# Kernel tuning notes

Measured on AMD Instinct MI355X. Metric: run time of the kernel, lower is better.

Reference implementation:

```python
import jax, jax.numpy as jnp
import numpy as np

B, L, G, N, K, E = 64, 512, 128, 32, 8, 65536
NTOK, D_TOK, H_DIR, NTL_INP, NHID, NREL = 10000, 64, 64, 32, 16, 16


def _bn(x, gamma, beta, eps=1e-5):
    # training-mode BatchNorm1d over axis 0; x: (n, C)
    mu = x.mean(0)
    var = x.var(0)
    return gamma * (x - mu) / jnp.sqrt(var + eps) + beta


def _lstm(x, w_ih, w_hh, b_ih, b_hh):
    # x: (B, T, D); torch gate order i, f, g, o
    nb = x.shape[0]
    H = w_hh.shape[1]
    def step(carry, xt):
        h, c = carry
        g = xt @ w_ih.T + b_ih + h @ w_hh.T + b_hh
        i, f, gg, o = jnp.split(g, 4, axis=-1)
        c = jax.nn.sigmoid(f) * c + jax.nn.sigmoid(i) * jnp.tanh(gg)
        h = jax.nn.sigmoid(o) * jnp.tanh(c)
        return (h, c), h
    init = (jnp.zeros((nb, H), x.dtype), jnp.zeros((nb, H), x.dtype))
    _, hs = jax.lax.scan(step, init, jnp.swapaxes(x, 0, 1))
    return jnp.swapaxes(hs, 0, 1)


def setup_inputs() -> dict:
    key = jax.random.key(0)
    ks = jax.random.split(key, 24)
    inp = {}
    inp['seq'] = jax.random.randint(ks[0], (B, L), 0, NTOK)
    inp['pos2grp'] = jax.random.randint(ks[1], (B, L), 0, G)
    inp['idx'] = jax.random.randint(ks[2], (B, N, K), 0, L)
    inp['u'] = jax.random.randint(ks[3], (E,), 0, B * N)
    inp['v'] = jax.random.randint(ks[4], (E,), 0, B * N)
    # parameters
    s = 1.0 / np.sqrt(H_DIR)
    inp['tok_emb'] = jax.random.normal(ks[5], (NTOK, D_TOK), jnp.float32)
    for tag, k0 in (('f', 6), ('b', 10)):
        inp[f'w_ih_{tag}'] = s * jax.random.normal(ks[k0], (4 * H_DIR, D_TOK), jnp.float32)
        inp[f'w_hh_{tag}'] = s * jax.random.normal(ks[k0 + 1], (4 * H_DIR, H_DIR), jnp.float32)
        inp[f'b_ih_{tag}'] = s * jax.random.normal(ks[k0 + 2], (4 * H_DIR,), jnp.float32)
        inp[f'b_hh_{tag}'] = s * jax.random.normal(ks[k0 + 3], (4 * H_DIR,), jnp.float32)
    inp['w_src'] = (1.0 / np.sqrt(2 * H_DIR)) * jax.random.normal(ks[14], (NTL_INP, 2 * H_DIR), jnp.float32)
    inp['b_src'] = jnp.zeros((NTL_INP,), jnp.float32)
    inp['w_dst'] = (1.0 / np.sqrt(2 * H_DIR)) * jax.random.normal(ks[15], (NTL_INP, 2 * H_DIR), jnp.float32)
    inp['b_dst'] = jnp.zeros((NTL_INP,), jnp.float32)
    inp['g_src'] = jnp.ones((NTL_INP,), jnp.float32)
    inp['be_src'] = jnp.zeros((NTL_INP,), jnp.float32)
    inp['g_dst'] = jnp.ones((NTL_INP,), jnp.float32)
    inp['be_dst'] = jnp.zeros((NTL_INP,), jnp.float32)
    inp['ntl_w'] = 0.001 * jax.random.normal(ks[16], (NREL, NHID, NTL_INP, NTL_INP), jnp.float32)
    inp['ntl_v'] = 0.001 * jax.random.normal(ks[17], (NREL, NHID, 2 * NTL_INP), jnp.float32)
    inp['ntl_b'] = jnp.zeros((NREL, NHID, 1), jnp.float32)
    inp['ntl_u'] = 0.001 * jax.random.normal(ks[18], (NREL, 1, NHID), jnp.float32)
    inp['ntl_g'] = jnp.ones((NREL * NHID,), jnp.float32)
    inp['ntl_be'] = jnp.zeros((NREL * NHID,), jnp.float32)
    return inp


def reference(seq, pos2grp, idx, u, v, tok_emb,
              w_ih_f, w_hh_f, b_ih_f, b_hh_f,
              w_ih_b, w_hh_b, b_ih_b, b_hh_b,
              w_src, b_src, w_dst, b_dst,
              g_src, be_src, g_dst, be_dst,
              ntl_w, ntl_v, ntl_b, ntl_u, ntl_g, ntl_be):
    # token embed + scatter-sum tokens -> groups
    x_tok = tok_emb[seq]                                   # (B, L, D)
    gid = (pos2grp + jnp.arange(B)[:, None] * G).reshape(-1)
    x_grp = jax.ops.segment_sum(x_tok.reshape(B * L, -1), gid,
                                num_segments=B * G).reshape(B, G, -1)
    # bidirectional LSTM over groups
    hf = _lstm(x_grp, w_ih_f, w_hh_f, b_ih_f, b_hh_f)
    hb = jnp.flip(_lstm(jnp.flip(x_grp, 1), w_ih_b, w_hh_b, b_ih_b, b_hh_b), 1)
    h_grp = jnp.concatenate([hf, hb], -1)                  # (B, G, 2H)
    # hierarchical gather + sum: node <- sum over K token positions' groups
    b_idx = jnp.arange(B)[:, None, None]
    g_idx = pos2grp[b_idx, idx]                            # (B, N, K)
    h = h_grp[b_idx, g_idx].sum(2).reshape(B * N, -1)      # (B*N, 2H)
    # edge endpoint projections + batchnorm
    hs = _bn(h[u] @ w_src.T + b_src, g_src, be_src)        # (E, ninp)
    ht = _bn(h[v] @ w_dst.T + b_dst, g_dst, be_dst)
    # Neural Tensor Layer
    linear = jnp.einsum('rhd,nd->rhn', ntl_v, jnp.concatenate([hs, ht], 1))
    bil = jnp.stack([
        jnp.einsum('nhj,nj->hn', jnp.einsum('ni,hij->nhj', hs, ntl_w[r]), ht)
        for r in range(NREL)], 0)                          # (R, H, E)
    z = bil + linear + ntl_b
    mu = z.mean(-1, keepdims=True)
    var = z.var(-1, keepdims=True)
    zn = ntl_g.reshape(NREL, NHID, 1) * (z - mu) / jnp.sqrt(var + 1e-5) \
         + ntl_be.reshape(NREL, NHID, 1)
    t = jnp.tanh(zn)
    logit = jnp.einsum('rh,rhn->nr', ntl_u[:, 0, :], t)    # (E, R)
    return logit
```

## Files before the change

### kernel.cpp

```cpp
#include <hip/hip_runtime.h>
#include <hip/hip_bf16.h>
#include <cstdint>

constexpr int B_   = 64;
constexpr int L_   = 512;
constexpr int G_   = 128;
constexpr int E_   = 65536;
constexpr int RH   = 256;
constexpr int M_   = 2048;
constexpr int JA   = 33;
constexpr int COLS = RH * JA;
constexpr int STRD = 36;
constexpr int K_   = 8;

#define DEV static __device__ __forceinline__

DEV float sigm(float x) { return 1.f / (1.f + __expf(-x)); }
DEV float tanh_fast(float x) {
    x = fminf(15.f, fmaxf(-15.f, x));
    float e = __expf(2.f * x);
    return (e - 1.f) / (e + 1.f);
}
DEV int rfl(int x) { return __builtin_amdgcn_readfirstlane(x); }

__global__ __launch_bounds__(256) void k_eh(const int* __restrict__ seq,
                                            const int* __restrict__ p2g,
                                            const float* __restrict__ emb,
                                            const int* __restrict__ u,
                                            const int* __restrict__ v,
                                            float* __restrict__ xg,
                                            int* __restrict__ cu, int* __restrict__ cv) {
    int blk = blockIdx.x;
    int t   = threadIdx.x;
    if (blk >= 64) {
        int n = (blk - 64) * 256 + t;
        atomicAdd(&cu[u[n]], 1);
        atomicAdd(&cv[v[n]], 1);
        return;
    }
    __shared__ float xgl[G_ * 64];
    for (int i = t; i < G_ * 64; i += 256) xgl[i] = 0.f;
    __syncthreads();
    int b = blk;
    int d = t & 63, part = t >> 6;
#pragma unroll 8
    for (int l = part; l < L_; l += 4) {
        int s = seq[b * L_ + l];
        int g = p2g[b * L_ + l];
        atomicAdd(&xgl[g * 64 + d], emb[s * 64 + d]);
    }
    __syncthreads();
    for (int i = t; i < G_ * 64; i += 256) xg[(size_t)b * G_ * 64 + i] = xgl[i];
}

__global__ __launch_bounds__(256) void k_pre(const float* __restrict__ xg,
                                             const float* __restrict__ wihf,
                                             const float* __restrict__ bihf,
                                             const float* __restrict__ bhhf,
                                             const float* __restrict__ wihb,
                                             const float* __restrict__ bihb,
                                             const float* __restrict__ bhhb,
                                             float* __restrict__ pre,
                                             const int* __restrict__ cu,
                                             int* __restrict__ ustart,
                                             int* __restrict__ ucursor) {
    int blk = blockIdx.x;
    int t   = threadIdx.x;
    if (blk == 512) {
        __shared__ int ps[256];
        int base = t * 8, run = 0;
        int c[8], loc[8];
#pragma unroll
        for (int i = 0; i < 8; i++) c[i] = cu[base + i];
#pragma unroll
        for (int i = 0; i < 8; i++) { loc[i] = run; run += c[i]; }
        ps[t] = run;
        __syncthreads();
        for (int off = 1; off < 256; off <<= 1) {
            int a = (t >= off) ? ps[t - off] : 0;
            __syncthreads();
            ps[t] += a;
            __syncthreads();
        }
        int ex = ps[t] - run;
#pragma unroll
        for (int i = 0; i < 8; i++) { ustart[base + i] = ex + loc[i]; ucursor[base + i] = ex + loc[i]; }
        if (t == 255) ustart[2048] = E_;
        return;
    }
    int dir = blk >> 8;
    const float* wih = dir ? wihb : wihf;
    float bias = dir ? (bihb[t] + bhhb[t]) : (bihf[t] + bhhf[t]);
    int r0 = (blk & 255) * 32;

    float4 wv[16];
#pragma unroll
    for (int c = 0; c < 16; c++) wv[c] = ((const float4*)(wih + t * 64))[c];

#pragma unroll 2
    for (int ml = 0; ml < 32; ml++) {
        const float* xr = xg + (size_t)(r0 + ml) * 64;
        float acc = bias;
#pragma unroll
        for (int c = 0; c < 16; c++) {
            float x0 = xr[4 * c], x1 = xr[4 * c + 1], x2 = xr[4 * c + 2], x3 = xr[4 * c + 3];
            acc += x0 * wv[c].x + x1 * wv[c].y + x2 * wv[c].z + x3 * wv[c].w;
        }
        pre[((size_t)dir * 8192 + r0 + ml) * 256 + t] = acc;
    }
}

__global__ __launch_bounds__(256, 1) void k_lstm(const float* __restrict__ pre,
                                                 const float* __restrict__ whh_f,
                                                 const float* __restrict__ whh_b,
                                                 float* __restrict__ hgrp,
                                                 const int* __restrict__ u,
                                                 const int* __restrict__ v,
                                                 int* __restrict__ ucursor,
                                                 int2* __restrict__ eonv) {
    int blk = blockIdx.x;
    int t   = threadIdx.x;
    if (blk >= 128) {
        int n = (blk - 128) * 256 + t;
        int pos = atomicAdd(&ucursor[u[n]], 1);
        eonv[pos] = make_int2(n, v[n]);
        return;
    }
    __shared__ __align__(16) float plds[64][256];
    __shared__ __align__(16) float hl[2][64];
    __shared__ float gl[256];
    int dir = blk >> 6;
    int b   = blk & 63;
    const float* whh = dir ? whh_b : whh_f;
    const float* src = pre + ((size_t)dir * 8192 + (size_t)b * G_) * 256;

    float4 wv[16];
#pragma unroll
    for (int c = 0; c < 16; c++) wv[c] = ((const float4*)(whh + t * 64))[c];

    {
        int base = dir ? 64 : 0;
        const float4* s4 = (const float4*)(src + (size_t)base * 256);
        float4* d4 = (float4*)&plds[0][0];
#pragma unroll
        for (int i = 0; i < 16; i++) d4[i * 256 + t] = s4[i * 256 + t];
    }
    if (t < 64) hl[0][t] = 0.f;
    float creg = 0.f;
    __syncthreads();
    int q = t >> 6;

    for (int half = 0; half < 2; half++) {
        if (half == 1) {
            int base = dir ? 0 : 64;
            const float4* s4 = (const float4*)(src + (size_t)base * 256);
            float4* d4 = (float4*)&plds[0][0];
#pragma unroll
            for (int i = 0; i < 16; i++) d4[i * 256 + t] = s4[i * 256 + t];
            __syncthreads();
        }
        for (int kk = 0; kk < 64; kk++) {
            int k = half * 64 + kk;
            int s = dir ? (G_ - 1 - k) : k;
            float p = plds[s & 63][t];
            const float4* hp = (const float4*)hl[k & 1];
            float a0 = p, a1 = 0.f, a2 = 0.f, a3 = 0.f;
#pragma unroll
            for (int c = 0; c < 16; c += 4) {
                float4 h0 = hp[c], h1 = hp[c + 1], h2 = hp[c + 2], h3 = hp[c + 3];
                a0 += h0.x * wv[c].x     + h0.y * wv[c].y     + h0.z * wv[c].z     + h0.w * wv[c].w;
                a1 += h1.x * wv[c + 1].x + h1.y * wv[c + 1].y + h1.z * wv[c + 1].z + h1.w * wv[c + 1].w;
                a2 += h2.x * wv[c + 2].x + h2.y * wv[c + 2].y + h2.z * wv[c + 2].z + h2.w * wv[c + 2].w;
                a3 += h3.x * wv[c + 3].x + h3.y * wv[c + 3].y + h3.z * wv[c + 3].z + h3.w * wv[c + 3].w;
            }
            float g = (a0 + a1) + (a2 + a3);
            gl[t] = (q == 2) ? tanh_fast(g) : sigm(g);
            __syncthreads();
            if (t < 64) {
                float ai = gl[t], af = gl[64 + t], ag = gl[128 + t], ao = gl[192 + t];
                float c2 = af * creg + ai * ag;
                float hh = ao * tanh_fast(c2);
                creg = c2;
                hl[(k + 1) & 1][t] = hh;
                hgrp[((size_t)(b * G_ + s)) * 128 + dir * 64 + t] = hh;
            }
            __syncthreads();
        }
    }
}

__global__ __launch_bounds__(128) void k_gather(const int* __restrict__ idx,
                                                const int* __restrict__ p2g,
                                                const float* __restrict__ hgrp,
                                                float* __restrict__ hnode) {
    int m = blockIdx.x;
    int d = threadIdx.x;
    int b = m >> 5;
    float acc = 0.f;
#pragma unroll
    for (int k = 0; k < K_; k++) {
        int l = idx[m * K_ + k];
        int g = p2g[b * L_ + l];
        acc += hgrp[((size_t)b * G_ + g) * 128 + d];
    }
    hnode[(size_t)m * 128 + d] = acc;
}

__global__ __launch_bounds__(256) void k_proj(const float* __restrict__ hnode,
                                              const float* __restrict__ wsrc,
                                              const float* __restrict__ bsrc,
                                              const float* __restrict__ wdst,
                                              const float* __restrict__ bdst,
                                              float* __restrict__ Ps, float* __restrict__ Pd) {
    int m0 = blockIdx.x * 8;
    int t  = threadIdx.x;
    int ml = t >> 5, o = t & 31;
    float4 sw[32], dw[32];
#pragma unroll
    for (int c = 0; c < 32; c++) {
        sw[c] = ((const float4*)(wsrc + (size_t)o * 128))[c];
        dw[c] = ((const float4*)(wdst + (size_t)o * 128))[c];
    }
    const float* hr = hnode + (size_t)(m0 + ml) * 128;
    float accS = bsrc[o], accD = bdst[o];
#pragma unroll
    for (int c = 0; c < 32; c++) {
        float x0 = hr[4 * c], x1 = hr[4 * c + 1], x2 = hr[4 * c + 2], x3 = hr[4 * c + 3];
        accS += x0 * sw[c].x + x1 * sw[c].y + x2 * sw[c].z + x3 * sw[c].w;
        accD += x0 * dw[c].x + x1 * dw[c].y + x2 * dw[c].z + x3 * dw[c].w;
    }
    Ps[(size_t)(m0 + ml) * 32 + o] = accS;
    Pd[(size_t)(m0 + ml) * 32 + o] = accD;
}

__global__ __launch_bounds__(256) void k_bnstat(const float* __restrict__ Ps,
                                                 const float* __restrict__ Pd,
                                                 const int* __restrict__ cu,
                                                 const int* __restrict__ cv,
                                                 float* __restrict__ bn_raw) {
    int side = blockIdx.x & 1, sl = blockIdx.x >> 1;
    const float* P  = side ? Pd : Ps;
    const int*   cn = side ? cv : cu;
    int t = threadIdx.x;
    int mp = t >> 5, o = t & 31;
    float s1 = 0.f, s2 = 0.f;
#pragma unroll
    for (int i = 0; i < 8; i++) {
        int m = sl * 64 + i * 8 + mp;
        float c = (float)cn[m];
        float x = P[(size_t)m * 32 + o];
        s1 += c * x;
        s2 += c * x * x;
    }
    __shared__ float r1[256], r2[256];
    r1[t] = s1; r2[t] = s2;
    __syncthreads();
    for (int off = 128; off >= 32; off >>= 1) {
        if (t < off) { r1[t] += r1[t + off]; r2[t] += r2[t + off]; }
        __syncthreads();
    }
    if (t < 32) {
        atomicAdd(&bn_raw[side * 64 + t], r1[t]);
        atomicAdd(&bn_raw[side * 64 + 32 + t], r2[t]);
    }
}

__global__ __launch_bounds__(256) void k_prep(const float* __restrict__ Ps,
                                              const float* __restrict__ Pd,
                                              const float* __restrict__ bn_raw,
                                              const float* __restrict__ gs,
                                              const float* __restrict__ bes,
                                              const float* __restrict__ gd,
                                              const float* __restrict__ bed,
                                              const float* __restrict__ ntlw,
                                              const float* __restrict__ ntlv,
                                              const float* __restrict__ ntlb,
                                              float* __restrict__ hsaug,
                                              float* __restrict__ htaug,
                                              float* __restrict__ waug) {
    int blk = blockIdx.x;
    int t   = threadIdx.x;
    constexpr float invE = 1.f / (float)E_;
    if (blk < 576) {
        int gid = blk * 256 + t;
        int m = gid / (2 * STRD), s2 = gid % (2 * STRD);
        if (s2 < STRD) {
            int i = s2;
            float val = 0.f;
            if (i < 32) {
                float mu  = bn_raw[i] * invE;
                float isd = rsqrtf(bn_raw[32 + i] * invE - mu * mu + 1e-5f);
                val = gs[i] * (Ps[(size_t)m * 32 + i] - mu) * isd + bes[i];
            } else if (i == 32) val = 1.f;
            hsaug[(size_t)m * STRD + i] = val;
        } else {
            int j = s2 - STRD;
            float val = 0.f;
            if (j < 32) {
                float mu  = bn_raw[64 + j] * invE;
                float isd = rsqrtf(bn_raw[96 + j] * invE - mu * mu + 1e-5f);
                val = gd[j] * (Pd[(size_t)m * 32 + j] - mu) * isd + bed[j];
            } else if (j == 32) val = 1.f;
            htaug[(size_t)m * STRD + j] = val;
        }
        return;
    }
    int gid = (blk - 576) * 256 + t;
    int i   = gid / COLS;
    int rem = gid - i * COLS;
    int rh  = rem / JA;
    int j   = rem - rh * JA;
    float val;
    if (i < 32) val = (j < 32) ? ntlw[((size_t)rh * 32 + i) * 32 + j] : ntlv[rh * 64 + i];
    else        val = (j < 32) ? ntlv[rh * 64 + 32 + j] : ntlb[rh];
    waug[(size_t)i * COLS + j * 256 + rh] = val;
}

__global__ __launch_bounds__(256) void k_agemm(const float* __restrict__ hsaug,
                                               const float* __restrict__ waug,
                                               __hip_bfloat16* __restrict__ A) {
    int mt = blockIdx.x;
    int j  = blockIdx.y;
    int t  = threadIdx.x;
    float w[JA];
#pragma unroll
    for (int i = 0; i < JA; i++) w[i] = waug[(size_t)i * COLS + j * 256 + t];

#pragma unroll 2
    for (int ml = 0; ml < 32; ml++) {
        const float* hr = hsaug + (size_t)(mt * 32 + ml) * STRD;
        float a0 = 0.f, a1 = 0.f;
#pragma unroll
        for (int i = 0; i < 32; i += 2) {
            a0 += hr[i] * w[i];
            a1 += hr[i + 1] * w[i + 1];
        }
        float acc = a0 + a1 + hr[32] * w[32];
        A[(size_t)(mt * 32 + ml) * COLS + j * 256 + t] = __float2bfloat16(acc);
    }
}

DEV void load_ht(float* d, const float* __restrict__ htaug, int vv) {
    const float* hp = htaug + (size_t)vv * STRD;
#pragma unroll
    for (int j = 0; j < JA; j++) d[j] = hp[j];
}
DEV void edge_compute(const float* av, const float* ht, int n, int t,
                      __hip_bfloat16* __restrict__ z, float& s1, float& s2) {
    float a0 = 0.f, a1 = 0.f;
#pragma unroll
    for (int j = 0; j < 32; j += 2) {
        a0 += av[j] * ht[j];
        a1 += av[j + 1] * ht[j + 1];
    }
    float acc = a0 + a1 + av[32] * ht[32];
    z[(size_t)n * 256 + t] = __float2bfloat16(acc);
    s1 += acc; s2 += acc * acc;
}

__global__ __launch_bounds__(256) void k_z(const __hip_bfloat16* __restrict__ A,
                                           const float* __restrict__ htaug,
                                           const int* __restrict__ ustart,
                                           const int2* __restrict__ eonv,
                                           __hip_bfloat16* __restrict__ z,
                                           float* __restrict__ zsum,
                                           float* __restrict__ zsq) {
    int t = threadIdx.x;
    float s1 = 0.f, s2 = 0.f;
    for (int ui = 0; ui < 4; ui++) {
        int uu = blockIdx.x * 4 + ui;
        float av[JA];
#pragma unroll
        for (int j = 0; j < JA; j++)
            av[j] = __bfloat162float(A[(size_t)uu * COLS + j * 256 + t]);
        int e0 = ustart[uu], e1 = ustart[uu + 1];
        if (e0 >= e1) continue;
        int e = e0;
        int2 q0 = eonv[e];
        int n0 = rfl(q0.x), v0 = rfl(q0.y);
        float ht0[JA]; load_ht(ht0, htaug, v0);
        int n1 = 0, v1 = 0; float ht1[JA];
        while (true) {
            if (e + 1 < e1) {
                int2 q = eonv[e + 1];
                n1 = rfl(q.x); v1 = rfl(q.y);
                load_ht(ht1, htaug, v1);
            }
            edge_compute(av, ht0, n0, t, z, s1, s2);
            if (++e >= e1) break;
            if (e + 1 < e1) {
                int2 q = eonv[e + 1];
                n0 = rfl(q.x); v0 = rfl(q.y);
                load_ht(ht0, htaug, v0);
            }
            edge_compute(av, ht1, n1, t, z, s1, s2);
            if (++e >= e1) break;
        }
    }
    atomicAdd(&zsum[t], s1);
    atomicAdd(&zsq[t], s2);
}

__global__ __launch_bounds__(256) void k_logit(const __hip_bfloat16* __restrict__ z,
                                               const float* __restrict__ zsum,
                                               const float* __restrict__ zsq,
                                               const float* __restrict__ ntlu,
                                               const float* __restrict__ ntlg,
                                               const float* __restrict__ ntlbe,
                                               float* __restrict__ out) {
    int t  = threadIdx.x;
    int n0 = blockIdx.x * 16;
    float mu  = zsum[t] / (float)E_;
    float var = zsq[t] / (float)E_ - mu * mu;
    float isd = rsqrtf(var + 1e-5f);
    float g   = ntlg[t],  be  = ntlbe[t];
    float uw  = ntlu[t];
    float zv[16];
#pragma unroll
    for (int nl = 0; nl < 16; nl++)
        zv[nl] = __bfloat162float(z[(size_t)(n0 + nl) * 256 + t]);
#pragma unroll 1
    for (int nl = 0; nl < 16; nl++) {
        float zn  = g * (zv[nl] - mu) * isd + be;
        float val = uw * tanh_fast(zn);
        val += __shfl_xor(val, 1);
        val += __shfl_xor(val, 2);
        val += __shfl_xor(val, 4);
        val += __shfl_xor(val, 8);
        if ((t & 15) == 0) out[(size_t)(n0 + nl) * 16 + (t >> 4)] = val;
    }
}

extern "C" void kernel_launch(void* const* d_in, const int* in_sizes, int n_in,
                              void* d_out, int out_size, void* d_ws, size_t ws_size,
                              hipStream_t stream) {
    const int*   seq   = (const int*)d_in[0];
    const int*   p2g   = (const int*)d_in[1];
    const int*   idx   = (const int*)d_in[2];
    const int*   u     = (const int*)d_in[3];
    const int*   v     = (const int*)d_in[4];
    const float* emb   = (const float*)d_in[5];
    const float* wihf  = (const float*)d_in[6];
    const float* whhf  = (const float*)d_in[7];
    const float* bihf  = (const float*)d_in[8];
    const float* bhhf  = (const float*)d_in[9];
    const float* wihb  = (const float*)d_in[10];
    const float* whhb  = (const float*)d_in[11];
    const float* bihb  = (const float*)d_in[12];
    const float* bhhb  = (const float*)d_in[13];
    const float* wsrc  = (const float*)d_in[14];
    const float* bsrc  = (const float*)d_in[15];
    const float* wdst  = (const float*)d_in[16];
    const float* bdst  = (const float*)d_in[17];
    const float* gs    = (const float*)d_in[18];
    const float* bes   = (const float*)d_in[19];
    const float* gd    = (const float*)d_in[20];
    const float* bed   = (const float*)d_in[21];
    const float* ntlw  = (const float*)d_in[22];
    const float* ntlv  = (const float*)d_in[23];
    const float* ntlb  = (const float*)d_in[24];
    const float* ntlu  = (const float*)d_in[25];
    const float* ntlg  = (const float*)d_in[26];
    const float* ntlbe = (const float*)d_in[27];
    float* out = (float*)d_out;

    char* ws = (char*)d_ws;
    size_t off = 0;
    auto take = [&](size_t bytes) -> char* {
        char* p = ws + off;
        off = (off + bytes + 255) & ~(size_t)255;
        return p;
    };
    int*   cnt_u  = (int*)  take(2048 * 4);
    int*   cnt_v  = (int*)  take(2048 * 4);
    float* zsum   = (float*)take(256 * 4);
    float* zsq    = (float*)take(256 * 4);
    float* bn_raw = (float*)take(128 * 4);
    size_t zero_bytes = off;
    float* x_grp   = (float*)take((size_t)B_ * G_ * 64 * 4);
    int*   ucursor = (int*)  take(2048 * 4);
    int*   ustart  = (int*)  take(2049 * 4);
    int2*  eonv    = (int2*) take((size_t)E_ * 8);
    float* pre     = (float*)take((size_t)2 * 8192 * 256 * 4);
    float* hgrp    = (float*)take((size_t)B_ * G_ * 128 * 4);
    float* hnode   = (float*)take((size_t)M_ * 128 * 4);
    float* Psrc    = (float*)take((size_t)M_ * 32 * 4);
    float* Pdst    = (float*)take((size_t)M_ * 32 * 4);
    float* hsaug   = (float*)take((size_t)M_ * STRD * 4);
    float* htaug   = (float*)take((size_t)M_ * STRD * 4);
    float* waug    = (float*)take((size_t)JA * COLS * 4);
    __hip_bfloat16* Abuf = (__hip_bfloat16*)take((size_t)M_ * COLS * 2);
    __hip_bfloat16* zbuf = (__hip_bfloat16*)take((size_t)E_ * 256 * 2);
    (void)ws_size; (void)in_sizes; (void)n_in; (void)out_size;

    hipMemsetAsync(d_ws, 0, zero_bytes, stream);

    k_eh<<<320, 256, 0, stream>>>(seq, p2g, emb, u, v, x_grp, cnt_u, cnt_v);
    k_pre<<<513, 256, 0, stream>>>(x_grp, wihf, bihf, bhhf, wihb, bihb, bhhb, pre,
                                   cnt_u, ustart, ucursor);
    k_lstm<<<384, 256, 0, stream>>>(pre, whhf, whhb, hgrp, u, v, ucursor, eonv);
    k_gather<<<M_, 128, 0, stream>>>(idx, p2g, hgrp, hnode);
    k_proj<<<M_ / 8, 256, 0, stream>>>(hnode, wsrc, bsrc, wdst, bdst, Psrc, Pdst);
    k_bnstat<<<64, 256, 0, stream>>>(Psrc, Pdst, cnt_u, cnt_v, bn_raw);
    k_prep<<<576 + 1089, 256, 0, stream>>>(Psrc, Pdst, bn_raw, gs, bes, gd, bed,
                                           ntlw, ntlv, ntlb, hsaug, htaug, waug);
    k_agemm<<<dim3(64, JA), 256, 0, stream>>>(hsaug, waug, Abuf);
    k_z<<<M_ / 4, 256, 0, stream>>>(Abuf, htaug, ustart, eonv, zbuf, zsum, zsq);
    k_logit<<<E_ / 16, 256, 0, stream>>>(zbuf, zsum, zsq, ntlu, ntlg, ntlbe, out);
}
```

Measured before the change: 428.9 us.

## Redo LSTM recurrence with lane broadcasts, fuse gather/proj/bnstat, widen k_z grid

The LSTM step now keeps h in registers and broadcasts it with readlane instead of going through LDS. Each wave redundantly computes the cell update, which removes the second barrier per step, and the h history is buffered in LDS then written out per half. The gather, projection and BN-statistics kernels are merged into one kernel that keeps the node rows in shared memory, removing the hnode round trip and two launches. k_z now launches one block per source node instead of four, giving more parallelism at the cost of more blocks and more per-block atomics.

```diff
diff --git a/kernel.cpp b/kernel.cpp
--- a/kernel.cpp
+++ b/kernel.cpp
@@ -11,7 +11,6 @@
 constexpr int JA   = 33;
 constexpr int COLS = RH * JA;
 constexpr int STRD = 36;
-constexpr int K_   = 8;
 
 #define DEV static __device__ __forceinline__
 
@@ -22,6 +21,9 @@
     return (e - 1.f) / (e + 1.f);
 }
 DEV int rfl(int x) { return __builtin_amdgcn_readfirstlane(x); }
+DEV float rdlane(float x, int lane) {
+    return __int_as_float(__builtin_amdgcn_readlane(__float_as_int(x), lane));
+}
 
 __global__ __launch_bounds__(256) void k_eh(const int* __restrict__ seq,
                                             const int* __restrict__ p2g,
@@ -127,141 +129,135 @@
         return;
     }
     __shared__ __align__(16) float plds[64][256];
-    __shared__ __align__(16) float hl[2][64];
-    __shared__ float gl[256];
+    __shared__ __align__(16) float hist[64][64];
+    __shared__ float gl[2][256];
     int dir = blk >> 6;
     int b   = blk & 63;
     const float* whh = dir ? whh_b : whh_f;
     const float* src = pre + ((size_t)dir * 8192 + (size_t)b * G_) * 256;
+    int e = t & 63;
+    int q = t >> 6;
 
     float4 wv[16];
 #pragma unroll
-    for (int c = 0; c < 16; c++) wv[c] = ((const float4*)(whh + t * 64))[c];
-
-    {
-        int base = dir ? 64 : 0;
-        const float4* s4 = (const float4*)(src + (size_t)base * 256);
-        float4* d4 = (float4*)&plds[0][0];
-#pragma unroll
-        for (int i = 0; i < 16; i++) d4[i * 256 + t] = s4[i * 256 + t];
-    }
-    if (t < 64) hl[0][t] = 0.f;
-    float creg = 0.f;
-    __syncthreads();
-    int q = t >> 6;
+    for (int c = 0; c < 16; c++) wv[c] = ((const float4*)(whh + (size_t)t * 64))[c];
+
+    float h = 0.f, creg = 0.f;
 
     for (int half = 0; half < 2; half++) {
-        if (half == 1) {
-            int base = dir ? 0 : 64;
+        {
+            int base = (dir ^ half) ? 64 : 0;
             const float4* s4 = (const float4*)(src + (size_t)base * 256);
             float4* d4 = (float4*)&plds[0][0];
 #pragma unroll
             for (int i = 0; i < 16; i++) d4[i * 256 + t] = s4[i * 256 + t];
-            __syncthreads();
-        }
+        }
+        __syncthreads();
         for (int kk = 0; kk < 64; kk++) {
             int k = half * 64 + kk;
-            int s = dir ? (G_ - 1 - k) : k;
-            float p = plds[s & 63][t];
-            const float4* hp = (const float4*)hl[k & 1];
+            int srow = dir ? (63 - kk) : kk;
+            float p = plds[srow][t];
             float a0 = p, a1 = 0.f, a2 = 0.f, a3 = 0.f;
 #pragma unroll
-            for (int c = 0; c < 16; c += 4) {
-                float4 h0 = hp[c], h1 = hp[c + 1], h2 = hp[c + 2], h3 = hp[c + 3];
-                a0 += h0.x * wv[c].x     + h0.y * wv[c].y     + h0.z * wv[c].z     + h0.w * wv[c].w;
-                a1 += h1.x * wv[c + 1].x + h1.y * wv[c + 1].y + h1.z * wv[c + 1].z + h1.w * wv[c + 1].w;
-                a2 += h2.x * wv[c + 2].x + h2.y * wv[c + 2].y + h2.z * wv[c + 2].z + h2.w * wv[c + 2].w;
-                a3 += h3.x * wv[c + 3].x + h3.y * wv[c + 3].y + h3.z * wv[c + 3].z + h3.w * wv[c + 3].w;
+            for (int c = 0; c < 16; c++) {
+                float f0 = rdlane(h, 4 * c + 0);
+                float f1 = rdlane(h, 4 * c + 1);
+                float f2 = rdlane(h, 4 * c + 2);
+                float f3 = rdlane(h, 4 * c + 3);
+                a0 += wv[c].x * f0;
+                a1 += wv[c].y * f1;
+                a2 += wv[c].z * f2;
+                a3 += wv[c].w * f3;
             }
             float g = (a0 + a1) + (a2 + a3);
-            gl[t] = (q == 2) ? tanh_fast(g) : sigm(g);
+            gl[k & 1][t] = (q == 2) ? tanh_fast(g) : sigm(g);
             __syncthreads();
-            if (t < 64) {
-                float ai = gl[t], af = gl[64 + t], ag = gl[128 + t], ao = gl[192 + t];
-                float c2 = af * creg + ai * ag;
-                float hh = ao * tanh_fast(c2);
-                creg = c2;
-                hl[(k + 1) & 1][t] = hh;
-                hgrp[((size_t)(b * G_ + s)) * 128 + dir * 64 + t] = hh;
-            }
-            __syncthreads();
-        }
-    }
-}
-
-__global__ __launch_bounds__(128) void k_gather(const int* __restrict__ idx,
-                                                const int* __restrict__ p2g,
-                                                const float* __restrict__ hgrp,
-                                                float* __restrict__ hnode) {
-    int m = blockIdx.x;
-    int d = threadIdx.x;
-    int b = m >> 5;
-    float acc = 0.f;
-#pragma unroll
-    for (int k = 0; k < K_; k++) {
-        int l = idx[m * K_ + k];
-        int g = p2g[b * L_ + l];
-        acc += hgrp[((size_t)b * G_ + g) * 128 + d];
-    }
-    hnode[(size_t)m * 128 + d] = acc;
-}
-
-__global__ __launch_bounds__(256) void k_proj(const float* __restrict__ hnode,
-                                              const float* __restrict__ wsrc,
-                                              const float* __restrict__ bsrc,
-                                              const float* __restrict__ wdst,
-                                              const float* __restrict__ bdst,
-                                              float* __restrict__ Ps, float* __restrict__ Pd) {
+            float ai = gl[k & 1][e];
+            float af = gl[k & 1][64 + e];
+            float ag = gl[k & 1][128 + e];
+            float ao = gl[k & 1][192 + e];
+            creg = af * creg + ai * ag;
+            h = ao * tanh_fast(creg);
+            if (q == 0) hist[srow][e] = h;
+        }
+        __syncthreads();
+        int sbase = (dir ? (1 - half) : half) * 64;
+#pragma unroll
+        for (int i = 0; i < 16; i++) {
+            int row = q * 16 + i;
+            int s = sbase + row;
+            hgrp[((size_t)(b * G_ + s)) * 128 + dir * 64 + e] = hist[row][e];
+        }
+    }
+}
+
+__global__ __launch_bounds__(256) void k_gp(const int* __restrict__ idx,
+                                            const int* __restrict__ p2g,
+                                            const float* __restrict__ hgrp,
+                                            const int* __restrict__ cu,
+                                            const int* __restrict__ cv,
+                                            const float* __restrict__ wsrc,
+                                            const float* __restrict__ bsrc,
+                                            const float* __restrict__ wdst,
+                                            const float* __restrict__ bdst,
+                                            float* __restrict__ Ps, float* __restrict__ Pd,
+                                            float* __restrict__ bn_raw) {
+    __shared__ __align__(16) float hsl[8][128];
+    __shared__ float red[256];
     int m0 = blockIdx.x * 8;
     int t  = threadIdx.x;
+    int d = t & 127, mh = t >> 7;
+#pragma unroll
+    for (int rep = 0; rep < 4; rep++) {
+        int ml = rep * 2 + mh;
+        int m  = m0 + ml;
+        int b  = m >> 5;
+        float acc = 0.f;
+#pragma unroll
+        for (int k = 0; k < 8; k++) {
+            int l = idx[m * 8 + k];
+            int g = p2g[b * L_ + l];
+            acc += hgrp[((size_t)b * G_ + g) * 128 + d];
+        }
+        hsl[ml][d] = acc;
+    }
+    __syncthreads();
     int ml = t >> 5, o = t & 31;
-    float4 sw[32], dw[32];
-#pragma unroll
-    for (int c = 0; c < 32; c++) {
-        sw[c] = ((const float4*)(wsrc + (size_t)o * 128))[c];
-        dw[c] = ((const float4*)(wdst + (size_t)o * 128))[c];
-    }
-    const float* hr = hnode + (size_t)(m0 + ml) * 128;
-    float accS = bsrc[o], accD = bdst[o];
-#pragma unroll
-    for (int c = 0; c < 32; c++) {
-        float x0 = hr[4 * c], x1 = hr[4 * c + 1], x2 = hr[4 * c + 2], x3 = hr[4 * c + 3];
-        accS += x0 * sw[c].x + x1 * sw[c].y + x2 * sw[c].z + x3 * sw[c].w;
-        accD += x0 * dw[c].x + x1 * dw[c].y + x2 * dw[c].z + x3 * dw[c].w;
-    }
-    Ps[(size_t)(m0 + ml) * 32 + o] = accS;
-    Pd[(size_t)(m0 + ml) * 32 + o] = accD;
-}
-
-__global__ __launch_bounds__(256) void k_bnstat(const float* __restrict__ Ps,
-                                                 const float* __restrict__ Pd,
-                                                 const int* __restrict__ cu,
-                                                 const int* __restrict__ cv,
-                                                 float* __restrict__ bn_raw) {
-    int side = blockIdx.x & 1, sl = blockIdx.x >> 1;
-    const float* P  = side ? Pd : Ps;
-    const int*   cn = side ? cv : cu;
-    int t = threadIdx.x;
-    int mp = t >> 5, o = t & 31;
-    float s1 = 0.f, s2 = 0.f;
-#pragma unroll
-    for (int i = 0; i < 8; i++) {
-        int m = sl * 64 + i * 8 + mp;
-        float c = (float)cn[m];
-        float x = P[(size_t)m * 32 + o];
-        s1 += c * x;
-        s2 += c * x * x;
-    }
-    __shared__ float r1[256], r2[256];
-    r1[t] = s1; r2[t] = s2;
-    __syncthreads();
-    for (int off = 128; off >= 32; off >>= 1) {
-        if (t < off) { r1[t] += r1[t + off]; r2[t] += r2[t + off]; }
-        __syncthreads();
-    }
-    if (t < 32) {
-        atomicAdd(&bn_raw[side * 64 + t], r1[t]);
-        atomicAdd(&bn_raw[side * 64 + 32 + t], r2[t]);
+    int m  = m0 + ml;
+    const float4* hp = (const float4*)&hsl[ml][0];
+    float cw_u = (float)cu[m], cw_v = (float)cv[m];
+#pragma unroll 1
+    for (int side = 0; side < 2; side++) {
+        const float* W = side ? wdst : wsrc;
+        float4 wr[32];
+#pragma unroll
+        for (int c = 0; c < 32; c++) wr[c] = ((const float4*)(W + (size_t)o * 128))[c];
+        float acc = side ? bdst[o] : bsrc[o];
+#pragma unroll
+        for (int c = 0; c < 32; c++) {
+            float4 h4 = hp[c];
+            acc += h4.x * wr[c].x + h4.y * wr[c].y + h4.z * wr[c].z + h4.w * wr[c].w;
+        }
+        (side ? Pd : Ps)[(size_t)m * 32 + o] = acc;
+        float cw = side ? cw_v : cw_u;
+        red[t] = cw * acc;
+        __syncthreads();
+        if (t < 32) {
+            float s = 0.f;
+#pragma unroll
+            for (int i = 0; i < 8; i++) s += red[i * 32 + t];
+            atomicAdd(&bn_raw[side * 64 + t], s);
+        }
+        __syncthreads();
+        red[t] = cw * acc * acc;
+        __syncthreads();
+        if (t < 32) {
+            float s = 0.f;
+#pragma unroll
+            for (int i = 0; i < 8; i++) s += red[i * 32 + t];
+            atomicAdd(&bn_raw[side * 64 + 32 + t], s);
+        }
+        __syncthreads();
     }
 }
 
@@ -365,33 +361,32 @@
                                            __hip_bfloat16* __restrict__ z,
                                            float* __restrict__ zsum,
                                            float* __restrict__ zsq) {
-    int t = threadIdx.x;
+    int t  = threadIdx.x;
+    int uu = blockIdx.x;
     float s1 = 0.f, s2 = 0.f;
-    for (int ui = 0; ui < 4; ui++) {
-        int uu = blockIdx.x * 4 + ui;
-        float av[JA];
-#pragma unroll
-        for (int j = 0; j < JA; j++)
-            av[j] = __bfloat162float(A[(size_t)uu * COLS + j * 256 + t]);
-        int e0 = ustart[uu], e1 = ustart[uu + 1];
-        if (e0 >= e1) continue;
+    float av[JA];
+#pragma unroll
+    for (int j = 0; j < JA; j++)
+        av[j] = __bfloat162float(A[(size_t)uu * COLS + j * 256 + t]);
+    int e0 = ustart[uu], e1 = ustart[uu + 1];
+    if (e0 < e1) {
         int e = e0;
         int2 q0 = eonv[e];
         int n0 = rfl(q0.x), v0 = rfl(q0.y);
         float ht0[JA]; load_ht(ht0, htaug, v0);
-        int n1 = 0, v1 = 0; float ht1[JA];
+        int n1 = 0; float ht1[JA];
         while (true) {
             if (e + 1 < e1) {
                 int2 q = eonv[e + 1];
-                n1 = rfl(q.x); v1 = rfl(q.y);
+                n1 = rfl(q.x); int v1 = rfl(q.y);
                 load_ht(ht1, htaug, v1);
             }
             edge_compute(av, ht0, n0, t, z, s1, s2);
             if (++e >= e1) break;
             if (e + 1 < e1) {
                 int2 q = eonv[e + 1];
-                n0 = rfl(q.x); v0 = rfl(q.y);
-                load_ht(ht0, htaug, v0);
+                n0 = rfl(q.x); int v0b = rfl(q.y);
+                load_ht(ht0, htaug, v0b);
             }
             edge_compute(av, ht1, n1, t, z, s1, s2);
             if (++e >= e1) break;
@@ -483,7 +478,6 @@
     int2*  eonv    = (int2*) take((size_t)E_ * 8);
     float* pre     = (float*)take((size_t)2 * 8192 * 256 * 4);
     float* hgrp    = (float*)take((size_t)B_ * G_ * 128 * 4);
-    float* hnode   = (float*)take((size_t)M_ * 128 * 4);
     float* Psrc    = (float*)take((size_t)M_ * 32 * 4);
     float* Pdst    = (float*)take((size_t)M_ * 32 * 4);
     float* hsaug   = (float*)take((size_t)M_ * STRD * 4);
@@ -499,12 +493,11 @@
     k_pre<<<513, 256, 0, stream>>>(x_grp, wihf, bihf, bhhf, wihb, bihb, bhhb, pre,
                                    cnt_u, ustart, ucursor);
     k_lstm<<<384, 256, 0, stream>>>(pre, whhf, whhb, hgrp, u, v, ucursor, eonv);
-    k_gather<<<M_, 128, 0, stream>>>(idx, p2g, hgrp, hnode);
-    k_proj<<<M_ / 8, 256, 0, stream>>>(hnode, wsrc, bsrc, wdst, bdst, Psrc, Pdst);
-    k_bnstat<<<64, 256, 0, stream>>>(Psrc, Pdst, cnt_u, cnt_v, bn_raw);
+    k_gp<<<M_ / 8, 256, 0, stream>>>(idx, p2g, hgrp, cnt_u, cnt_v,
+                                     wsrc, bsrc, wdst, bdst, Psrc, Pdst, bn_raw);
     k_prep<<<576 + 1089, 256, 0, stream>>>(Psrc, Pdst, bn_raw, gs, bes, gd, bed,
                                            ntlw, ntlv, ntlb, hsaug, htaug, waug);
     k_agemm<<<dim3(64, JA), 256, 0, stream>>>(hsaug, waug, Abuf);
-    k_z<<<M_ / 4, 256, 0, stream>>>(Abuf, htaug, ustart, eonv, zbuf, zsum, zsq);
+    k_z<<<M_, 256, 0, stream>>>(Abuf, htaug, ustart, eonv, zbuf, zsum, zsq);
     k_logit<<<E_ / 16, 256, 0, stream>>>(zbuf, zsum, zsq, ntlu, ntlg, ntlbe, out);
 }
```

Measured after the change: 417.5 us. 1.03x faster.
